# Kernel tuning notes

Measured on AMD Instinct MI355X. Metric: run time of the kernel, lower is better.

Reference implementation:

```python
import jax, jax.numpy as jnp
import numpy as np

B, H, S, D = 2, 16, 2048, 128


def setup_inputs() -> dict:
    key = jax.random.key(0)
    kq, kk, kv = jax.random.split(key, 3)
    q = jax.random.normal(kq, (B, H, S, D), dtype=jnp.float32)
    k = jax.random.normal(kk, (B, H, S, D), dtype=jnp.float32)
    v = jax.random.normal(kv, (B, H, S, D), dtype=jnp.float32)
    return {"q": q, "k": k, "v": v}


def reference(q, k, v):
    # cp_size == 1 path: causal scaled dot-product attention.
    # Identical math to the ring online-softmax accumulation collapsed to one step.
    d = q.shape[-1]
    scale = d ** -0.5
    scores = jnp.einsum("bhsd,bhtd->bhst", q, k) * scale  # (B,H,S,S)
    s = scores.shape[-1]
    causal_mask = jnp.tril(jnp.ones((s, s), dtype=bool))  # (S,S)
    scores = jnp.where(causal_mask, scores, -jnp.inf)
    probs = jax.nn.softmax(scores, axis=-1)
    return jnp.einsum("bhst,bhtd->bhsd", probs, v)
```

## Files before the change

kernel.cpp:

```cpp
#include <hip/hip_runtime.h>
#include <hip/hip_bf16.h>

constexpr int Bb = 2, Hh = 16, Ss = 2048, Dd = 128;
constexpr int BM = 64, BN = 64;
constexpr int NQT = Ss / BM;
constexpr float SCALE = 0.088388347648318447f;

typedef __attribute__((ext_vector_type(8))) short bf16x8;
typedef __attribute__((ext_vector_type(4))) float f32x4;
typedef __attribute__((ext_vector_type(4))) int int4v;

__device__ __forceinline__ unsigned bfbits(float f) {
  union { float f; unsigned u; } v; v.f = f;
  return v.u + 0x7FFFu + ((v.u >> 16) & 1u);
}
__device__ __forceinline__ short f2bf(float f) { return (short)(bfbits(f) >> 16); }
__device__ __forceinline__ unsigned packbf(float lo, float hi) {
  return (bfbits(lo) >> 16) | (bfbits(hi) & 0xFFFF0000u);
}
__device__ __forceinline__ float fcomp(float4 f, int j) {
  return j == 0 ? f.x : (j == 1 ? f.y : (j == 2 ? f.z : f.w));
}

__global__ __launch_bounds__(256, 2)
void fa_fwd_kernel(const float* __restrict__ q, const float* __restrict__ k,
                   const float* __restrict__ v, float* __restrict__ out) {
  __shared__ __align__(16) char Klds[BN * 256];
  __shared__ __align__(16) char Vlds[Dd * 128];

  const int tid = threadIdx.x;
  const int wave = tid >> 6, lane = tid & 63, quad = lane >> 4, l16 = lane & 15;
  const int bid = blockIdx.x;
  const int bh = bid & 31;
  const int qt = (NQT - 1) - (bid >> 5);

  const float* qb = q + (size_t)bh * Ss * Dd;
  const float* kb = k + (size_t)bh * Ss * Dd;
  const float* vb = v + (size_t)bh * Ss * Dd;

  bf16x8 qf[4];
  {
    const float* qr = qb + (size_t)(qt * BM + wave * 16 + l16) * Dd + quad * 8;
    #pragma unroll
    for (int ks = 0; ks < 4; ++ks) {
      float4 a = *(const float4*)(qr + ks * 32);
      float4 b = *(const float4*)(qr + ks * 32 + 4);
      bf16x8 t;
      t[0]=f2bf(a.x*SCALE); t[1]=f2bf(a.y*SCALE); t[2]=f2bf(a.z*SCALE); t[3]=f2bf(a.w*SCALE);
      t[4]=f2bf(b.x*SCALE); t[5]=f2bf(b.y*SCALE); t[6]=f2bf(b.z*SCALE); t[7]=f2bf(b.w*SCALE);
      qf[ks] = t;
    }
  }

  const int krow0 = tid >> 4;
  const int kblk  = tid & 15;
  const int kswz  = kblk ^ krow0;
  const int vkg = tid >> 5;
  const int vdq = tid & 31;

  float4 ka[4], kc[4];
  float4 vr[8];

  auto load_tiles = [&](int kt) {
    const float* Kg = kb + (size_t)(kt * BN) * Dd + kblk * 8;
    #pragma unroll
    for (int i = 0; i < 4; ++i) {
      ka[i] = *(const float4*)(Kg + (size_t)(krow0 + 16 * i) * Dd);
      kc[i] = *(const float4*)(Kg + (size_t)(krow0 + 16 * i) * Dd + 4);
    }
    const float* Vg = vb + (size_t)(kt * BN + vkg * 8) * Dd + vdq * 4;
    #pragma unroll
    for (int r = 0; r < 8; ++r)
      vr[r] = *(const float4*)(Vg + (size_t)r * Dd);
  };

  auto stage_tiles = [&]() {
    #pragma unroll
    for (int i = 0; i < 4; ++i) {
      bf16x8 t;
      t[0]=f2bf(ka[i].x); t[1]=f2bf(ka[i].y); t[2]=f2bf(ka[i].z); t[3]=f2bf(ka[i].w);
      t[4]=f2bf(kc[i].x); t[5]=f2bf(kc[i].y); t[6]=f2bf(kc[i].z); t[7]=f2bf(kc[i].w);
      *(bf16x8*)(Klds + (krow0 + 16 * i) * 256 + kswz * 16) = t;
    }
    #pragma unroll
    for (int j = 0; j < 4; ++j) {
      int d = vdq * 4 + j;
      int f7 = (d ^ (d >> 3)) & 7;
      bf16x8 t;
      #pragma unroll
      for (int r = 0; r < 8; ++r) t[r] = f2bf(fcomp(vr[r], j));
      *(bf16x8*)(Vlds + d * 128 + (vkg ^ f7) * 16) = t;
    }
  };

  f32x4 o[8];
  #pragma unroll
  for (int i = 0; i < 8; ++i) o[i] = (f32x4)(0.0f);
  float mrow = -3.0e38f, lrow = 0.0f;

  load_tiles(0);
  stage_tiles();

  const int hi2 = quad >> 1;
  const int srcbase = (l16 + 32 * (quad & 1)) * 4;

  for (int kt = 0; kt <= qt; ++kt) {
    __syncthreads();
    const bool more = kt < qt;
    if (more) load_tiles(kt + 1);

    f32x4 acc[4];
    #pragma unroll
    for (int nt = 0; nt < 4; ++nt) acc[nt] = (f32x4)(0.0f);
    #pragma unroll
    for (int ks = 0; ks < 4; ++ks) {
      #pragma unroll
      for (int nt = 0; nt < 4; ++nt) {
        int row = nt * 16 + l16;
        int bswz = (ks * 4 + quad) ^ l16;
        bf16x8 kf = *(const bf16x8*)(Klds + row * 256 + bswz * 16);
        acc[nt] = __builtin_amdgcn_mfma_f32_16x16x32_bf16(kf, qf[ks], acc[nt], 0, 0, 0);
      }
    }

    if (kt == qt) {
      #pragma unroll
      for (int nt = 0; nt < 4; ++nt)
        #pragma unroll
        for (int r = 0; r < 4; ++r)
          if (nt * 16 + quad * 4 + r > wave * 16 + l16) acc[nt][r] = -1.0e30f;
    }

    float mx = acc[0][0];
    #pragma unroll
    for (int nt = 0; nt < 4; ++nt)
      #pragma unroll
      for (int r = 0; r < 4; ++r) mx = fmaxf(mx, acc[nt][r]);
    mx = fmaxf(mx, __shfl_xor(mx, 16, 64));
    mx = fmaxf(mx, __shfl_xor(mx, 32, 64));
    float mn = fmaxf(mrow, mx);
    float alpha = __expf(mrow - mn);
    mrow = mn;
    float rs = 0.f;
    #pragma unroll
    for (int nt = 0; nt < 4; ++nt)
      #pragma unroll
      for (int r = 0; r < 4; ++r) {
        float p = __expf(acc[nt][r] - mn);
        acc[nt][r] = p; rs += p;
      }
    rs += __shfl_xor(rs, 16, 64);
    rs += __shfl_xor(rs, 32, 64);
    lrow = lrow * alpha + rs;

    unsigned pk0_0 = packbf(acc[0][0], acc[0][1]), pk0_1 = packbf(acc[0][2], acc[0][3]);
    unsigned pk1_0 = packbf(acc[1][0], acc[1][1]), pk1_1 = packbf(acc[1][2], acc[1][3]);
    unsigned pk2_0 = packbf(acc[2][0], acc[2][1]), pk2_1 = packbf(acc[2][2], acc[2][3]);
    unsigned pk3_0 = packbf(acc[3][0], acc[3][1]), pk3_1 = packbf(acc[3][2], acc[3][3]);

    #pragma unroll
    for (int r = 0; r < 4; ++r) {
      int src = (lane & 48) | (quad * 4 + r);
      float ar = __shfl(alpha, src, 64);
      #pragma unroll
      for (int dt = 0; dt < 8; ++dt) o[dt][r] *= ar;
    }

    bf16x8 pf[2];
    {
      int4v p0, p1;
      #pragma unroll
      for (int jp = 0; jp < 4; ++jp) {
        int srcb = srcbase + 64 * (jp >> 1);
        int a0 = __builtin_amdgcn_ds_bpermute(srcb, (int)((jp & 1) ? pk0_1 : pk0_0));
        int a1 = __builtin_amdgcn_ds_bpermute(srcb, (int)((jp & 1) ? pk1_1 : pk1_0));
        int a2 = __builtin_amdgcn_ds_bpermute(srcb, (int)((jp & 1) ? pk2_1 : pk2_0));
        int a3 = __builtin_amdgcn_ds_bpermute(srcb, (int)((jp & 1) ? pk3_1 : pk3_0));
        p0[jp] = hi2 ? a1 : a0;
        p1[jp] = hi2 ? a3 : a2;
      }
      pf[0] = __builtin_bit_cast(bf16x8, p0);
      pf[1] = __builtin_bit_cast(bf16x8, p1);
    }

    #pragma unroll
    for (int ks2 = 0; ks2 < 2; ++ks2) {
      #pragma unroll
      for (int dt = 0; dt < 8; ++dt) {
        int row = dt * 16 + l16;
        int f7 = (row ^ (row >> 3)) & 7;
        int bswz = (ks2 * 4 + quad) ^ f7;
        bf16x8 vf = *(const bf16x8*)(Vlds + row * 128 + bswz * 16);
        o[dt] = __builtin_amdgcn_mfma_f32_16x16x32_bf16(pf[ks2], vf, o[dt], 0, 0, 0);
      }
    }

    if (more) { __syncthreads(); stage_tiles(); }
  }

  float linv[4];
  #pragma unroll
  for (int r = 0; r < 4; ++r) {
    int src = (lane & 48) | (quad * 4 + r);
    linv[r] = 1.0f / __shfl(lrow, src, 64);
  }
  float* ob = out + ((size_t)bh * Ss + qt * BM + wave * 16) * Dd;
  #pragma unroll
  for (int dt = 0; dt < 8; ++dt)
    #pragma unroll
    for (int r = 0; r < 4; ++r)
      ob[(quad * 4 + r) * Dd + dt * 16 + l16] = o[dt][r] * linv[r];
}

extern "C" void kernel_launch(void* const* d_in, const int* in_sizes, int n_in,
                              void* d_out, int out_size, void* d_ws, size_t ws_size,
                              hipStream_t stream) {
  const float* q = (const float*)d_in[0];
  const float* k = (const float*)d_in[1];
  const float* v = (const float*)d_in[2];
  float* out = (float*)d_out;
  dim3 grid(Bb * Hh * NQT);
  dim3 block(256);
  hipLaunchKernelGGL(fa_fwd_kernel, grid, block, 0, stream, q, k, v, out);
}
```

Baseline: 205.0 us.

## Use padded LDS layout, exp2 softmax, packed bf16 converts and conditional rescale

Replaces the XOR-swizzled K/V shared-memory layouts with padded row strides, so the read addresses become simple constant offsets from a precomputed base pointer. Folds log2(e) into the Q scale and switches to a hardware exp2, and uses a packed bf16 conversion builtin where available. Skips the output rescale when no row maximum grew in the wave, and raises the launch bound to three blocks per SM. In exchange it uses slightly more LDS per block and adds register pressure under the tighter occupancy bound, and the V staging thread mapping changes.

```diff
diff --git a/kernel.cpp b/kernel.cpp
--- a/kernel.cpp
+++ b/kernel.cpp
@@ -4,7 +4,10 @@
 constexpr int Bb = 2, Hh = 16, Ss = 2048, Dd = 128;
 constexpr int BM = 64, BN = 64;
 constexpr int NQT = Ss / BM;
-constexpr float SCALE = 0.088388347648318447f;
+constexpr float SCALE = 0.088388347648318447f * 1.4426950408889634f;
+
+constexpr int KSTRIDE = 272;
+constexpr int VSTRIDE = 144;
 
 typedef __attribute__((ext_vector_type(8))) short bf16x8;
 typedef __attribute__((ext_vector_type(4))) float f32x4;
@@ -14,19 +17,31 @@
   union { float f; unsigned u; } v; v.f = f;
   return v.u + 0x7FFFu + ((v.u >> 16) & 1u);
 }
-__device__ __forceinline__ short f2bf(float f) { return (short)(bfbits(f) >> 16); }
-__device__ __forceinline__ unsigned packbf(float lo, float hi) {
-  return (bfbits(lo) >> 16) | (bfbits(hi) & 0xFFFF0000u);
+__device__ __forceinline__ unsigned pkbf(float lo, float hi) {
+#if __has_builtin(__builtin_amdgcn_cvt_pk_bf16_f32)
+  typedef __attribute__((ext_vector_type(2))) __bf16 bf16x2;
+  bf16x2 r = __builtin_amdgcn_cvt_pk_bf16_f32(lo, hi);
+  return __builtin_bit_cast(unsigned, r);
+#else
+  return __builtin_amdgcn_perm(bfbits(hi), bfbits(lo), 0x07060302u);
+#endif
+}
+__device__ __forceinline__ float exp2fast(float x) {
+#if __has_builtin(__builtin_amdgcn_exp2f)
+  return __builtin_amdgcn_exp2f(x);
+#else
+  return exp2f(x);
+#endif
 }
 __device__ __forceinline__ float fcomp(float4 f, int j) {
   return j == 0 ? f.x : (j == 1 ? f.y : (j == 2 ? f.z : f.w));
 }
 
-__global__ __launch_bounds__(256, 2)
+__global__ __launch_bounds__(256, 3)
 void fa_fwd_kernel(const float* __restrict__ q, const float* __restrict__ k,
                    const float* __restrict__ v, float* __restrict__ out) {
-  __shared__ __align__(16) char Klds[BN * 256];
-  __shared__ __align__(16) char Vlds[Dd * 128];
+  __shared__ __align__(16) char Klds[BN * KSTRIDE];
+  __shared__ __align__(16) char Vlds[Dd * VSTRIDE];
 
   const int tid = threadIdx.x;
   const int wave = tid >> 6, lane = tid & 63, quad = lane >> 4, l16 = lane & 15;
@@ -45,18 +60,16 @@
     for (int ks = 0; ks < 4; ++ks) {
       float4 a = *(const float4*)(qr + ks * 32);
       float4 b = *(const float4*)(qr + ks * 32 + 4);
-      bf16x8 t;
-      t[0]=f2bf(a.x*SCALE); t[1]=f2bf(a.y*SCALE); t[2]=f2bf(a.z*SCALE); t[3]=f2bf(a.w*SCALE);
-      t[4]=f2bf(b.x*SCALE); t[5]=f2bf(b.y*SCALE); t[6]=f2bf(b.z*SCALE); t[7]=f2bf(b.w*SCALE);
-      qf[ks] = t;
+      int4v t = { (int)pkbf(a.x*SCALE, a.y*SCALE), (int)pkbf(a.z*SCALE, a.w*SCALE),
+                  (int)pkbf(b.x*SCALE, b.y*SCALE), (int)pkbf(b.z*SCALE, b.w*SCALE) };
+      qf[ks] = __builtin_bit_cast(bf16x8, t);
     }
   }
 
   const int krow0 = tid >> 4;
   const int kblk  = tid & 15;
-  const int kswz  = kblk ^ krow0;
-  const int vkg = tid >> 5;
-  const int vdq = tid & 31;
+  const int vdq = tid >> 3;
+  const int vkg = tid & 7;
 
   float4 ka[4], kc[4];
   float4 vr[8];
@@ -77,19 +90,18 @@
   auto stage_tiles = [&]() {
     #pragma unroll
     for (int i = 0; i < 4; ++i) {
-      bf16x8 t;
-      t[0]=f2bf(ka[i].x); t[1]=f2bf(ka[i].y); t[2]=f2bf(ka[i].z); t[3]=f2bf(ka[i].w);
-      t[4]=f2bf(kc[i].x); t[5]=f2bf(kc[i].y); t[6]=f2bf(kc[i].z); t[7]=f2bf(kc[i].w);
-      *(bf16x8*)(Klds + (krow0 + 16 * i) * 256 + kswz * 16) = t;
+      int4v t = { (int)pkbf(ka[i].x, ka[i].y), (int)pkbf(ka[i].z, ka[i].w),
+                  (int)pkbf(kc[i].x, kc[i].y), (int)pkbf(kc[i].z, kc[i].w) };
+      *(int4v*)(Klds + (krow0 + 16 * i) * KSTRIDE + kblk * 16) = t;
     }
     #pragma unroll
     for (int j = 0; j < 4; ++j) {
       int d = vdq * 4 + j;
-      int f7 = (d ^ (d >> 3)) & 7;
-      bf16x8 t;
-      #pragma unroll
-      for (int r = 0; r < 8; ++r) t[r] = f2bf(fcomp(vr[r], j));
-      *(bf16x8*)(Vlds + d * 128 + (vkg ^ f7) * 16) = t;
+      int4v t = { (int)pkbf(fcomp(vr[0], j), fcomp(vr[1], j)),
+                  (int)pkbf(fcomp(vr[2], j), fcomp(vr[3], j)),
+                  (int)pkbf(fcomp(vr[4], j), fcomp(vr[5], j)),
+                  (int)pkbf(fcomp(vr[6], j), fcomp(vr[7], j)) };
+      *(int4v*)(Vlds + d * VSTRIDE + vkg * 16) = t;
     }
   };
 
@@ -103,6 +115,8 @@
 
   const int hi2 = quad >> 1;
   const int srcbase = (l16 + 32 * (quad & 1)) * 4;
+  const char* Krd = Klds + l16 * KSTRIDE + quad * 16;
+  const char* Vrd = Vlds + l16 * VSTRIDE + quad * 16;
 
   for (int kt = 0; kt <= qt; ++kt) {
     __syncthreads();
@@ -116,9 +130,7 @@
     for (int ks = 0; ks < 4; ++ks) {
       #pragma unroll
       for (int nt = 0; nt < 4; ++nt) {
-        int row = nt * 16 + l16;
-        int bswz = (ks * 4 + quad) ^ l16;
-        bf16x8 kf = *(const bf16x8*)(Klds + row * 256 + bswz * 16);
+        bf16x8 kf = *(const bf16x8*)(Krd + nt * (16 * KSTRIDE) + ks * 64);
         acc[nt] = __builtin_amdgcn_mfma_f32_16x16x32_bf16(kf, qf[ks], acc[nt], 0, 0, 0);
       }
     }
@@ -139,32 +151,34 @@
     mx = fmaxf(mx, __shfl_xor(mx, 16, 64));
     mx = fmaxf(mx, __shfl_xor(mx, 32, 64));
     float mn = fmaxf(mrow, mx);
-    float alpha = __expf(mrow - mn);
+    float alpha = 1.0f;
+    if (__any(mx > mrow)) {
+      alpha = exp2fast(mrow - mn);
+      #pragma unroll
+      for (int r = 0; r < 4; ++r) {
+        int src = (lane & 48) | (quad * 4 + r);
+        float ar = __shfl(alpha, src, 64);
+        #pragma unroll
+        for (int dt = 0; dt < 8; ++dt) o[dt][r] *= ar;
+      }
+    }
     mrow = mn;
     float rs = 0.f;
     #pragma unroll
     for (int nt = 0; nt < 4; ++nt)
       #pragma unroll
       for (int r = 0; r < 4; ++r) {
-        float p = __expf(acc[nt][r] - mn);
+        float p = exp2fast(acc[nt][r] - mn);
         acc[nt][r] = p; rs += p;
       }
     rs += __shfl_xor(rs, 16, 64);
     rs += __shfl_xor(rs, 32, 64);
     lrow = lrow * alpha + rs;
 
-    unsigned pk0_0 = packbf(acc[0][0], acc[0][1]), pk0_1 = packbf(acc[0][2], acc[0][3]);
-    unsigned pk1_0 = packbf(acc[1][0], acc[1][1]), pk1_1 = packbf(acc[1][2], acc[1][3]);
-    unsigned pk2_0 = packbf(acc[2][0], acc[2][1]), pk2_1 = packbf(acc[2][2], acc[2][3]);
-    unsigned pk3_0 = packbf(acc[3][0], acc[3][1]), pk3_1 = packbf(acc[3][2], acc[3][3]);
-
-    #pragma unroll
-    for (int r = 0; r < 4; ++r) {
-      int src = (lane & 48) | (quad * 4 + r);
-      float ar = __shfl(alpha, src, 64);
-      #pragma unroll
-      for (int dt = 0; dt < 8; ++dt) o[dt][r] *= ar;
-    }
+    unsigned pk0_0 = pkbf(acc[0][0], acc[0][1]), pk0_1 = pkbf(acc[0][2], acc[0][3]);
+    unsigned pk1_0 = pkbf(acc[1][0], acc[1][1]), pk1_1 = pkbf(acc[1][2], acc[1][3]);
+    unsigned pk2_0 = pkbf(acc[2][0], acc[2][1]), pk2_1 = pkbf(acc[2][2], acc[2][3]);
+    unsigned pk3_0 = pkbf(acc[3][0], acc[3][1]), pk3_1 = pkbf(acc[3][2], acc[3][3]);
 
     bf16x8 pf[2];
     {
@@ -187,10 +201,7 @@
     for (int ks2 = 0; ks2 < 2; ++ks2) {
       #pragma unroll
       for (int dt = 0; dt < 8; ++dt) {
-        int row = dt * 16 + l16;
-        int f7 = (row ^ (row >> 3)) & 7;
-        int bswz = (ks2 * 4 + quad) ^ f7;
-        bf16x8 vf = *(const bf16x8*)(Vlds + row * 128 + bswz * 16);
+        bf16x8 vf = *(const bf16x8*)(Vrd + dt * (16 * VSTRIDE) + ks2 * 64);
         o[dt] = __builtin_amdgcn_mfma_f32_16x16x32_bf16(pf[ks2], vf, o[dt], 0, 0, 0);
       }
     }
```

Measured after the change: 214.8 us. +4.7%, slower.
